# Kernel tuning notes

Hardware: AMD Instinct MI355X
Metric: run time of the kernel (lower is better)

Reference implementation:

```python
import jax, jax.numpy as jnp
import numpy as np

H = 16  # nhead


def setup_inputs() -> dict:
    key = jax.random.key(0)
    ks = jax.random.split(key, 10)
    B, N, D = 2, 2048, 1024
    n_ctx = 1024
    P = 256
    s = lambda fan: 1.0 / np.sqrt(fan)
    return {
        "x": jax.random.normal(ks[0], (B, N, D), jnp.float32),
        "n_ctx": n_ctx,
        "ctx_ppr": jax.random.uniform(ks[1], (n_ctx,), jnp.float32),
        "ctx_delta": jax.random.normal(ks[2], (n_ctx, P), jnp.float32),
        "ctx_trust": jax.random.normal(ks[3], (n_ctx,), jnp.float32),
        "W_in": jax.random.normal(ks[4], (3 * D, D), jnp.float32) * s(D),
        "b_in": jnp.zeros((3 * D,), jnp.float32),
        "W_out": jax.random.normal(ks[5], (D, D), jnp.float32) * s(D),
        "b_out": jnp.zeros((D,), jnp.float32),
        "log_ppr_alpha": jnp.full((1,), 0.1, jnp.float32),
        "trust_scale": jnp.full((1,), 0.1, jnp.float32),
        "Wd1": jax.random.normal(ks[6], (D // 2, P), jnp.float32) * s(P),
        "bd1": jnp.zeros((D // 2,), jnp.float32),
        "Wd2": jax.random.normal(ks[7], (1, D // 2), jnp.float32) * 0.01,
        "bd2": jnp.zeros((1,), jnp.float32),
    }


def reference(x, n_ctx, ctx_ppr, ctx_delta, ctx_trust, W_in, b_in, W_out, b_out,
              log_ppr_alpha, trust_scale, Wd1, bd1, Wd2, bd2):
    B, N, D = x.shape
    d = D // H
    scale = d ** -0.5

    qkv = x @ W_in.T + b_in                       # [B,N,3D]
    q, k, v = jnp.split(qkv, 3, axis=-1)
    to_heads = lambda t: t.reshape(B, N, H, d).transpose(0, 2, 1, 3)  # [B,H,N,d]
    q, k, v = to_heads(q), to_heads(k), to_heads(v)

    # sigmoid value gate on context keys
    gate = jax.nn.sigmoid(trust_scale * ctx_trust)           # [n_ctx]
    gate_full = jnp.concatenate([gate, jnp.ones(N - n_ctx, x.dtype)])
    v = v * gate_full[None, None, :, None]

    logits = jnp.einsum('bhqd,bhkd->bhqk', q, k) * scale     # [B,H,N,N]

    # additive per-key bias: alpha*log(ppr) + delta MLP
    ppr_bias = log_ppr_alpha * jnp.log(jnp.clip(ctx_ppr, 1e-8))
    h = jax.nn.gelu(ctx_delta @ Wd1.T + bd1, approximate=False)
    delta_bias = (h @ Wd2.T + bd2)[:, 0]                     # [n_ctx]
    col_bias = jnp.concatenate([ppr_bias + delta_bias, jnp.zeros(N - n_ctx, x.dtype)])
    logits = logits + col_bias[None, None, None, :]

    weights = jax.nn.softmax(logits, axis=-1)
    out = jnp.einsum('bhqk,bhkd->bhqd', weights, v)
    out = out.transpose(0, 2, 1, 3).reshape(B, N, D)
    return out @ W_out.T + b_out
```

## Files before the change

kernel.cpp:

```cpp
#include <hip/hip_runtime.h>
#include <hip/hip_bf16.h>
#include <hip/hip_fp16.h>
#include <math.h>


#define NTOK 2048
#define DMODEL 1024
#define NHEAD 16
#define DHEAD 64
#define NCTX 1024
#define BTOT 4096

typedef __attribute__((ext_vector_type(8))) _Float16 h8v;
typedef __attribute__((ext_vector_type(4))) float    f4v;
typedef __attribute__((ext_vector_type(4))) ushort   us4;
typedef __attribute__((ext_vector_type(8))) ushort   us8;

__device__ __forceinline__ ushort f2h(float x) {
    return __half_as_ushort(__float2half_rn(x));
}

#define GLDS16(gsrc, ldst) __builtin_amdgcn_global_load_lds(                              \
    (__attribute__((address_space(1))) unsigned int*)(gsrc),                              \
    (__attribute__((address_space(3))) unsigned int*)(ldst), 16, 0, 0)

__global__ __launch_bounds__(256)
void bias_kernel(const float* __restrict__ ctx_ppr, const float* __restrict__ ctx_delta,
                 const float* __restrict__ ctx_trust,
                 const float* __restrict__ alpha, const float* __restrict__ tscale,
                 const float* __restrict__ Wd1, const float* __restrict__ bd1,
                 const float* __restrict__ Wd2, const float* __restrict__ bd2,
                 float* __restrict__ gate_full, float* __restrict__ col_bias)
{
    const int i = blockIdx.x;
    const int t = threadIdx.x;
    if (i >= NCTX) {
        if (t == 0) { gate_full[i] = 1.0f; col_bias[i] = 0.0f; }
        return;
    }
    __shared__ float drow[256];
    __shared__ float red[256];
    drow[t] = ctx_delta[i * 256 + t];
    __syncthreads();

    float partial = 0.0f;
    #pragma unroll
    for (int jj = 0; jj < 2; jj++) {
        const int j = t + jj * 256;
        float s = bd1[j];
        const float4* wrow = (const float4*)&Wd1[j * 256];
        const float4* dr   = (const float4*)drow;
        #pragma unroll 8
        for (int p = 0; p < 64; p++) {
            float4 w = wrow[p], dd = dr[p];
            s += w.x * dd.x + w.y * dd.y + w.z * dd.z + w.w * dd.w;
        }
        float g = 0.5f * s * (1.0f + erff(s * 0.70710678118654752f));
        partial += g * Wd2[j];
    }
    red[t] = partial;
    __syncthreads();
    for (int off = 128; off > 0; off >>= 1) {
        if (t < off) red[t] += red[t + off];
        __syncthreads();
    }
    if (t == 0) {
        float ppr = fmaxf(ctx_ppr[i], 1e-8f);
        col_bias[i]  = alpha[0] * logf(ppr) + (red[0] + bd2[0]);
        gate_full[i] = 1.0f / (1.0f + __expf(-(tscale[0] * ctx_trust[i])));
    }
}

__global__ __launch_bounds__(256)
void cvt_all(const float* __restrict__ x, const float* __restrict__ wi,
             const float* __restrict__ wo,
             ushort* __restrict__ xf, ushort* __restrict__ wif, ushort* __restrict__ wof)
{
    for (int i = blockIdx.x * 256 + threadIdx.x; i < 2097152; i += gridDim.x * 256) {
        const float* src; ushort* dst; int j;
        if (i < 1048576)      { src = x;  dst = xf;  j = i; }
        else if (i < 1835008) { src = wi; dst = wif; j = i - 1048576; }
        else                  { src = wo; dst = wof; j = i - 1835008; }
        float4 v = ((const float4*)src)[j];
        us4 h;
        h[0] = f2h(v.x); h[1] = f2h(v.y); h[2] = f2h(v.z); h[3] = f2h(v.w);
        ((us4*)dst)[j] = h;
    }
}

template<int MT, int EPI>
__global__ __launch_bounds__(256, 3)
void gemm_f16(const ushort* __restrict__ Af, const ushort* __restrict__ Bf,
              const float* __restrict__ bias, float* __restrict__ C,
              ushort* __restrict__ qf, ushort* __restrict__ kf,
              ushort* __restrict__ vtf,
              const float* __restrict__ gate_full, int M, int N, int K)
{
    constexpr int BM = MT * 32;
    __shared__ ushort AS[BM * 32], BS[4096];

    const int t = threadIdx.x, lane = t & 63, wid = t >> 6;
    const int l15 = lane & 15, l4 = lane >> 4;
    const int wr = wid >> 1, wc = wid & 1;

    const int nwg = gridDim.x * gridDim.y;
    const int lin = blockIdx.y * gridDim.x + blockIdx.x;
    const int w   = (lin & 7) * (nwg >> 3) + (lin >> 3);
    const int bx  = w % gridDim.x, by = w / gridDim.x;
    const int m0 = by * BM, n0 = bx * 128;

    f4v acc[MT][4];
    #pragma unroll
    for (int mi = 0; mi < MT; mi++)
        #pragma unroll
        for (int nj = 0; nj < 4; nj++)
            #pragma unroll
            for (int r = 0; r < 4; r++) acc[mi][nj][r] = 0.0f;

    const int srow_l = lane >> 2;
    const int schunk = (lane & 3) ^ ((lane >> 2) & 3) ^ ((lane >> 4) & 3);
    const int rch = l4 ^ (l15 & 3) ^ ((l15 >> 2) & 3);

    for (int k0 = 0; k0 < K; k0 += 32) {
        __syncthreads();
        if (wid < 2) {
            #pragma unroll
            for (int i = 0; i < MT; i++) {
                const int row = (wid & 1) * (MT * 16) + i * 16 + srow_l;
                GLDS16(Af + (size_t)(m0 + row) * K + k0 + schunk * 8,
                       AS + ((wid & 1) * MT + i) * 512);
            }
        } else {
            #pragma unroll
            for (int i = 0; i < 4; i++) {
                const int row = (wid & 1) * 64 + i * 16 + srow_l;
                GLDS16(Bf + (size_t)(n0 + row) * K + k0 + schunk * 8,
                       BS + ((wid & 1) * 4 + i) * 512);
            }
        }
        __syncthreads();

        h8v af[MT], bf[4];
        #pragma unroll
        for (int mi = 0; mi < MT; mi++) {
            const int row = wr * (MT * 16) + mi * 16 + l15;
            af[mi] = *(const h8v*)&AS[row * 32 + rch * 8];
        }
        #pragma unroll
        for (int nj = 0; nj < 4; nj++) {
            const int row = wc * 64 + nj * 16 + l15;
            bf[nj] = *(const h8v*)&BS[row * 32 + rch * 8];
        }
        #pragma unroll
        for (int mi = 0; mi < MT; mi++)
            #pragma unroll
            for (int nj = 0; nj < 4; nj++)
                acc[mi][nj] = __builtin_amdgcn_mfma_f32_16x16x32_f16(af[mi], bf[nj], acc[mi][nj], 0, 0, 0);
    }

    if (EPI == 0) {
        #pragma unroll
        for (int mi = 0; mi < MT; mi++) {
            #pragma unroll
            for (int nj = 0; nj < 4; nj++) {
                const int n = n0 + wc * 64 + nj * 16 + l15;
                const float bn = bias[n];
                #pragma unroll
                for (int r = 0; r < 4; r++) {
                    const int m = m0 + wr * (MT * 16) + mi * 16 + l4 * 4 + r;
                    C[(size_t)m * N + n] = acc[mi][nj][r] + bn;
                }
            }
        }
    } else {
        const int sec = n0 >> 10;
        #pragma unroll
        for (int mi = 0; mi < MT; mi++) {
            const int mbase = m0 + wr * (MT * 16) + mi * 16 + l4 * 4;
            const int bb = mbase >> 11, tok0 = mbase & 2047;
            #pragma unroll
            for (int nj = 0; nj < 4; nj++) {
                const int n = n0 + wc * 64 + nj * 16 + l15;
                const float bn = bias[n];
                const int rem = n & 1023, h = rem >> 6, jd = rem & 63;
                if (sec == 2) {
                    us4 hv;
                    #pragma unroll
                    for (int r = 0; r < 4; r++)
                        hv[r] = f2h((acc[mi][nj][r] + bn) * gate_full[tok0 + r]);
                    const size_t vb = ((size_t)((bb << 4) + h) * 64 + jd) * NTOK + tok0;
                    *(us4*)&vtf[vb] = hv;
                } else {
                    ushort* dst = sec ? kf : qf;
                    #pragma unroll
                    for (int r = 0; r < 4; r++) {
                        const size_t idx = ((size_t)((bb << 4) + h) * NTOK + (tok0 + r)) * 64 + jd;
                        dst[idx] = f2h(acc[mi][nj][r] + bn);
                    }
                }
            }
        }
    }
}

__global__ __launch_bounds__(256, 4)
void attn_f16(const ushort* __restrict__ qfp, const ushort* __restrict__ kfp,
              const ushort* __restrict__ vtf, const float* __restrict__ col_bias,
              ushort* __restrict__ attf)
{
    __shared__ ushort KS[2][4096];
    __shared__ ushort VS[2][4096];
    __shared__ float  CBS[2][64];

    const int t = threadIdx.x, lane = t & 63, wid = t >> 6;
    const int lin = blockIdx.y * gridDim.x + blockIdx.x;
    const int w   = (lin & 7) * 128 + (lin >> 3);
    const int bh  = w >> 5, qt = w & 31;

    const size_t qkbase = (size_t)bh * (NTOK * DHEAD);
    const size_t vtbase = (size_t)bh * (DHEAD * NTOK);
    const int l15 = lane & 15, l4 = lane >> 4;
    const int q0 = qt * 64 + wid * 16;

    h8v qf[2];
    #pragma unroll
    for (int s = 0; s < 2; s++)
        qf[s] = *(const h8v*)&qfp[qkbase + (size_t)(q0 + l15) * 64 + 32 * s + 8 * l4];

    f4v oacc[4];
    #pragma unroll
    for (int f = 0; f < 4; f++)
        #pragma unroll
        for (int r = 0; r < 4; r++) oacc[f][r] = 0.0f;
    float mreg = -INFINITY;
    float sreg = 0.0f;

    us8 vreg[4];
    const int vj = lane & 7, vdh0 = lane >> 3;
    const int k0c  = 4 * (vj >> 2) + 2 * (vj & 1);
    const int off0 = ((vj >> 1) & 1) * 8;

    #define STAGE_K(nb, kt) do {                                                          \
        _Pragma("unroll")                                                                 \
        for (int i_ = 0; i_ < 4; i_++) {                                                  \
            const int row_ = wid * 32 + i_ * 8 + (lane >> 3);                             \
            const int sc_  = ((lane & 7) ^ (row_ & 7)) * 8;                               \
            GLDS16(kfp + qkbase + (size_t)((kt) + row_) * 64 + sc_,                       \
                   &KS[nb][0] + (wid * 4 + i_) * 512);                                    \
        }                                                                                 \
        if (wid == 0 && lane < 16) GLDS16(col_bias + (kt) + lane * 4, &CBS[nb][0]);       \
    } while (0)

    #define LOAD_V(kt) do {                                                               \
        _Pragma("unroll")                                                                 \
        for (int i_ = 0; i_ < 4; i_++) {                                                  \
            const int dh_ = (wid - 2) * 32 + 8 * i_ + vdh0;                               \
            vreg[i_] = *(const us8*)&vtf[vtbase + (size_t)dh_ * NTOK + (kt) + 8 * vj];    \
        }                                                                                 \
    } while (0)

    #define STORE_V(nb) do {                                                              \
        char* dp_ = (char*)&VS[nb][0];                                                    \
        _Pragma("unroll")                                                                 \
        for (int i_ = 0; i_ < 4; i_++) {                                                  \
            const int dh_ = (wid - 2) * 32 + 8 * i_ + vdh0;                               \
            const int b0_ = dh_ * 128 + ((k0c ^ (dh_ & 7)) * 16) + off0;                  \
            const int b1_ = dh_ * 128 + (((k0c + 1) ^ (dh_ & 7)) * 16) + off0;            \
            us4 lo4_, hi4_;                                                               \
            lo4_[0] = vreg[i_][0]; lo4_[1] = vreg[i_][1];                                 \
            lo4_[2] = vreg[i_][2]; lo4_[3] = vreg[i_][3];                                 \
            hi4_[0] = vreg[i_][4]; hi4_[1] = vreg[i_][5];                                 \
            hi4_[2] = vreg[i_][6]; hi4_[3] = vreg[i_][7];                                 \
            *(us4*)(dp_ + b0_) = lo4_;                                                    \
            *(us4*)(dp_ + b1_) = hi4_;                                                    \
        }                                                                                 \
    } while (0)

    if (wid < 2) STAGE_K(0, 0); else { LOAD_V(0); STORE_V(0); }
    __syncthreads();

    int cur = 0;
    for (int kt = 0; kt < 32; kt++) {
        const int nxt = cur ^ 1;
        if (kt < 31) { if (wid < 2) STAGE_K(nxt, (kt + 1) * 64); else LOAD_V((kt + 1) * 64); }

        f4v sa[4];
        #pragma unroll
        for (int g = 0; g < 4; g++)
            #pragma unroll
            for (int r = 0; r < 4; r++) sa[g][r] = 0.0f;
        __builtin_amdgcn_s_setprio(1);
        #pragma unroll
        for (int s = 0; s < 2; s++) {
            #pragma unroll
            for (int g = 0; g < 4; g++) {
                const int row = 16 * g + l15;
                const int idx = row * 64 + (((4 * s + l4) ^ (l15 & 7))) * 8;
                h8v kfr = *(const h8v*)&KS[cur][idx];
                sa[g] = __builtin_amdgcn_mfma_f32_16x16x32_f16(kfr, qf[s], sa[g], 0, 0, 0);
            }
        }
        __builtin_amdgcn_s_setprio(0);

        float sv[4][4], smax = -INFINITY;
        #pragma unroll
        for (int g = 0; g < 4; g++)
            #pragma unroll
            for (int r = 0; r < 4; r++) {
                const float x = sa[g][r] * 0.125f + CBS[cur][16 * g + 4 * l4 + r];
                sv[g][r] = x;
                smax = fmaxf(smax, x);
            }
        if (__any(smax > mreg + 8.0f)) {
            float mx = smax;
            mx = fmaxf(mx, __shfl_xor(mx, 16));
            mx = fmaxf(mx, __shfl_xor(mx, 32));
            const float mnew = fmaxf(mreg, mx);
            const float fs = __expf(mreg - mnew);
            mreg = mnew;
            sreg *= fs;
            float fq[4];
            #pragma unroll
            for (int r = 0; r < 4; r++) fq[r] = __shfl(fs, 4 * l4 + r);
            #pragma unroll
            for (int f = 0; f < 4; f++)
                #pragma unroll
                for (int r = 0; r < 4; r++) oacc[f][r] *= fq[r];
        }

        union H8 { h8v v; __half2 h2[4]; };
        H8 pa[2];
        {
            float pv[4][4];
            float acc_s = 0.0f;
            #pragma unroll
            for (int g = 0; g < 4; g++)
                #pragma unroll
                for (int r = 0; r < 4; r++) {
                    const float p = __expf(sv[g][r] - mreg);
                    pv[g][r] = p;
                    acc_s += p;
                }
            sreg += acc_s;
            #pragma unroll
            for (int s = 0; s < 2; s++)
                #pragma unroll
                for (int a = 0; a < 2; a++) {
                    const int g = 2 * s + a;
                    pa[s].h2[2 * a]     = __float22half2_rn(make_float2(pv[g][0], pv[g][1]));
                    pa[s].h2[2 * a + 1] = __float22half2_rn(make_float2(pv[g][2], pv[g][3]));
                }
        }

        __builtin_amdgcn_s_setprio(1);
        #pragma unroll
        for (int s = 0; s < 2; s++) {
            #pragma unroll
            for (int f = 0; f < 4; f++) {
                const int row = 16 * f + l15;
                const int idx = row * 64 + (((4 * s + l4) ^ (l15 & 7))) * 8;
                h8v vfr = *(const h8v*)&VS[cur][idx];
                oacc[f] = __builtin_amdgcn_mfma_f32_16x16x32_f16(pa[s].v, vfr, oacc[f], 0, 0, 0);
            }
        }
        __builtin_amdgcn_s_setprio(0);

        if (kt < 31 && wid >= 2) STORE_V(nxt);
        __syncthreads();
        cur = nxt;
    }

    const int b = bh >> 4, h = bh & 15;
    {
        float ts = sreg;
        ts += __shfl_xor(ts, 16);
        ts += __shfl_xor(ts, 32);
        const float inv = 1.0f / ts;
        float invq[4];
        #pragma unroll
        for (int r = 0; r < 4; r++) invq[r] = __shfl(inv, 4 * l4 + r);
        #pragma unroll
        for (int r = 0; r < 4; r++) {
            const int q = q0 + 4 * l4 + r;
            const size_t o = ((size_t)(b * NTOK + q)) * DMODEL + h * DHEAD + l15;
            #pragma unroll
            for (int f = 0; f < 4; f++)
                attf[o + 16 * f] = f2h(oacc[f][r] * invq[r]);
        }
    }
    #undef STAGE_K
    #undef LOAD_V
    #undef STORE_V
}

extern "C" void kernel_launch(void* const* d_in, const int* in_sizes, int n_in,
                              void* d_out, int out_size, void* d_ws, size_t ws_size,
                              hipStream_t stream)
{
    const float* x         = (const float*)d_in[0];
    const float* ctx_ppr   = (const float*)d_in[2];
    const float* ctx_delta = (const float*)d_in[3];
    const float* ctx_trust = (const float*)d_in[4];
    const float* W_in      = (const float*)d_in[5];
    const float* b_in      = (const float*)d_in[6];
    const float* W_out     = (const float*)d_in[7];
    const float* b_out     = (const float*)d_in[8];
    const float* alpha     = (const float*)d_in[9];
    const float* tscale    = (const float*)d_in[10];
    const float* Wd1       = (const float*)d_in[11];
    const float* bd1       = (const float*)d_in[12];
    const float* Wd2       = (const float*)d_in[13];
    const float* bd2       = (const float*)d_in[14];
    float* out = (float*)d_out;

    float* ws = (float*)d_ws;
    float* gate_full = ws;
    float* col_bias  = ws + 2048;
    ushort* u = (ushort*)(ws + 4096);
    ushort* xf   = u;  u += 4194304;
    ushort* wif  = u;  u += 3145728;
    ushort* wof  = u;  u += 1048576;
    ushort* qf   = u;  u += 4194304;
    ushort* kf   = u;  u += 4194304;
    ushort* vtf  = u;  u += 4194304;
    ushort* attf = u;  u += 4194304;

    bias_kernel<<<NTOK, 256, 0, stream>>>(ctx_ppr, ctx_delta, ctx_trust, alpha, tscale,
                                          Wd1, bd1, Wd2, bd2, gate_full, col_bias);
    cvt_all<<<2048, 256, 0, stream>>>(x, W_in, W_out, xf, wif, wof);

    gemm_f16<4, 1><<<dim3(24, 32), 256, 0, stream>>>(xf, wif, b_in, nullptr,
                                                     qf, kf, vtf, gate_full,
                                                     BTOT, 3 * DMODEL, DMODEL);
    attn_f16<<<dim3(32, 32), 256, 0, stream>>>(qf, kf, vtf, col_bias, attf);
    gemm_f16<2, 0><<<dim3(8, 64), 256, 0, stream>>>(attf, wof, b_out, out,
                                                    nullptr, nullptr, nullptr, nullptr,
                                                    BTOT, DMODEL, DMODEL);
}
```

Baseline: 275.2 us.

## Use exp2 softmax, MFMA row sums, trimmed bias launch, smaller out-proj tiles

```diff
diff --git a/kernel.cpp b/kernel.cpp
--- a/kernel.cpp
+++ b/kernel.cpp
@@ -10,6 +10,7 @@
 #define DHEAD 64
 #define NCTX 1024
 #define BTOT 4096
+#define LOG2E 1.4426950408889634f
 
 typedef __attribute__((ext_vector_type(8))) _Float16 h8v;
 typedef __attribute__((ext_vector_type(4))) float    f4v;
@@ -19,6 +20,12 @@
 __device__ __forceinline__ ushort f2h(float x) {
     return __half_as_ushort(__float2half_rn(x));
 }
+
+#if __has_builtin(__builtin_amdgcn_exp2f)
+#define EXP2F(x) __builtin_amdgcn_exp2f(x)
+#else
+#define EXP2F(x) exp2f(x)
+#endif
 
 #define GLDS16(gsrc, ldst) __builtin_amdgcn_global_load_lds(                              \
     (__attribute__((address_space(1))) unsigned int*)(gsrc),                              \
@@ -34,10 +41,6 @@
 {
     const int i = blockIdx.x;
     const int t = threadIdx.x;
-    if (i >= NCTX) {
-        if (t == 0) { gate_full[i] = 1.0f; col_bias[i] = 0.0f; }
-        return;
-    }
     __shared__ float drow[256];
     __shared__ float red[256];
     drow[t] = ctx_delta[i * 256 + t];
@@ -66,7 +69,7 @@
     }
     if (t == 0) {
         float ppr = fmaxf(ctx_ppr[i], 1e-8f);
-        col_bias[i]  = alpha[0] * logf(ppr) + (red[0] + bd2[0]);
+        col_bias[i]  = (alpha[0] * logf(ppr) + (red[0] + bd2[0])) * LOG2E;
         gate_full[i] = 1.0f / (1.0f + __expf(-(tscale[0] * ctx_trust[i])));
     }
 }
@@ -74,8 +77,16 @@
 __global__ __launch_bounds__(256)
 void cvt_all(const float* __restrict__ x, const float* __restrict__ wi,
              const float* __restrict__ wo,
-             ushort* __restrict__ xf, ushort* __restrict__ wif, ushort* __restrict__ wof)
+             ushort* __restrict__ xf, ushort* __restrict__ wif, ushort* __restrict__ wof,
+             float* __restrict__ gate_full, float* __restrict__ col_bias)
 {
+    if (blockIdx.x == 0) {
+        #pragma unroll
+        for (int j = threadIdx.x; j < NTOK - NCTX; j += 256) {
+            gate_full[NCTX + j] = 1.0f;
+            col_bias[NCTX + j]  = 0.0f;
+        }
+    }
     for (int i = blockIdx.x * 256 + threadIdx.x; i < 2097152; i += gridDim.x * 256) {
         const float* src; ushort* dst; int j;
         if (i < 1048576)      { src = x;  dst = xf;  j = i; }
@@ -227,13 +238,18 @@
     for (int s = 0; s < 2; s++)
         qf[s] = *(const h8v*)&qfp[qkbase + (size_t)(q0 + l15) * 64 + 32 * s + 8 * l4];
 
-    f4v oacc[4];
+    h8v vone;
+    #pragma unroll
+    for (int i = 0; i < 8; i++) vone[i] = (_Float16)1.0f;
+
+    f4v oacc[4], lsum;
     #pragma unroll
     for (int f = 0; f < 4; f++)
         #pragma unroll
         for (int r = 0; r < 4; r++) oacc[f][r] = 0.0f;
+    #pragma unroll
+    for (int r = 0; r < 4; r++) lsum[r] = 0.0f;
     float mreg = -INFINITY;
-    float sreg = 0.0f;
 
     us8 vreg[4];
     const int vj = lane & 7, vdh0 = lane >> 3;
@@ -302,26 +318,28 @@
         }
         __builtin_amdgcn_s_setprio(0);
 
+        const float SC2 = 0.125f * LOG2E;
         float sv[4][4], smax = -INFINITY;
         #pragma unroll
         for (int g = 0; g < 4; g++)
             #pragma unroll
             for (int r = 0; r < 4; r++) {
-                const float x = sa[g][r] * 0.125f + CBS[cur][16 * g + 4 * l4 + r];
+                const float x = sa[g][r] * SC2 + CBS[cur][16 * g + 4 * l4 + r];
                 sv[g][r] = x;
                 smax = fmaxf(smax, x);
             }
-        if (__any(smax > mreg + 8.0f)) {
+        if (__any(smax > mreg + 11.5415605f)) {
             float mx = smax;
             mx = fmaxf(mx, __shfl_xor(mx, 16));
             mx = fmaxf(mx, __shfl_xor(mx, 32));
             const float mnew = fmaxf(mreg, mx);
-            const float fs = __expf(mreg - mnew);
+            const float fs = EXP2F(mreg - mnew);
             mreg = mnew;
-            sreg *= fs;
             float fq[4];
             #pragma unroll
             for (int r = 0; r < 4; r++) fq[r] = __shfl(fs, 4 * l4 + r);
+            #pragma unroll
+            for (int r = 0; r < 4; r++) lsum[r] *= fq[r];
             #pragma unroll
             for (int f = 0; f < 4; f++)
                 #pragma unroll
@@ -332,16 +350,11 @@
         H8 pa[2];
         {
             float pv[4][4];
-            float acc_s = 0.0f;
             #pragma unroll
             for (int g = 0; g < 4; g++)
                 #pragma unroll
-                for (int r = 0; r < 4; r++) {
-                    const float p = __expf(sv[g][r] - mreg);
-                    pv[g][r] = p;
-                    acc_s += p;
-                }
-            sreg += acc_s;
+                for (int r = 0; r < 4; r++)
+                    pv[g][r] = EXP2F(sv[g][r] - mreg);
             #pragma unroll
             for (int s = 0; s < 2; s++)
                 #pragma unroll
@@ -355,6 +368,7 @@
         __builtin_amdgcn_s_setprio(1);
         #pragma unroll
         for (int s = 0; s < 2; s++) {
+            lsum = __builtin_amdgcn_mfma_f32_16x16x32_f16(pa[s].v, vone, lsum, 0, 0, 0);
             #pragma unroll
             for (int f = 0; f < 4; f++) {
                 const int row = 16 * f + l15;
@@ -371,22 +385,14 @@
     }
 
     const int b = bh >> 4, h = bh & 15;
-    {
-        float ts = sreg;
-        ts += __shfl_xor(ts, 16);
-        ts += __shfl_xor(ts, 32);
-        const float inv = 1.0f / ts;
-        float invq[4];
-        #pragma unroll
-        for (int r = 0; r < 4; r++) invq[r] = __shfl(inv, 4 * l4 + r);
-        #pragma unroll
-        for (int r = 0; r < 4; r++) {
-            const int q = q0 + 4 * l4 + r;
-            const size_t o = ((size_t)(b * NTOK + q)) * DMODEL + h * DHEAD + l15;
-            #pragma unroll
-            for (int f = 0; f < 4; f++)
-                attf[o + 16 * f] = f2h(oacc[f][r] * invq[r]);
-        }
+    #pragma unroll
+    for (int r = 0; r < 4; r++) {
+        const float inv = 1.0f / lsum[r];
+        const int q = q0 + 4 * l4 + r;
+        const size_t o = ((size_t)(b * NTOK + q)) * DMODEL + h * DHEAD + l15;
+        #pragma unroll
+        for (int f = 0; f < 4; f++)
+            attf[o + 16 * f] = f2h(oacc[f][r] * inv);
     }
     #undef STAGE_K
     #undef LOAD_V
@@ -425,15 +431,15 @@
     ushort* vtf  = u;  u += 4194304;
     ushort* attf = u;  u += 4194304;
 
-    bias_kernel<<<NTOK, 256, 0, stream>>>(ctx_ppr, ctx_delta, ctx_trust, alpha, tscale,
+    bias_kernel<<<NCTX, 256, 0, stream>>>(ctx_ppr, ctx_delta, ctx_trust, alpha, tscale,
                                           Wd1, bd1, Wd2, bd2, gate_full, col_bias);
-    cvt_all<<<2048, 256, 0, stream>>>(x, W_in, W_out, xf, wif, wof);
+    cvt_all<<<2048, 256, 0, stream>>>(x, W_in, W_out, xf, wif, wof, gate_full, col_bias);
 
     gemm_f16<4, 1><<<dim3(24, 32), 256, 0, stream>>>(xf, wif, b_in, nullptr,
                                                      qf, kf, vtf, gate_full,
                                                      BTOT, 3 * DMODEL, DMODEL);
     attn_f16<<<dim3(32, 32), 256, 0, stream>>>(qf, kf, vtf, col_bias, attf);
-    gemm_f16<2, 0><<<dim3(8, 64), 256, 0, stream>>>(attf, wof, b_out, out,
-                                                    nullptr, nullptr, nullptr, nullptr,
-                                                    BTOT, DMODEL, DMODEL);
-}
+    gemm_f16<1, 0><<<dim3(8, 128), 256, 0, stream>>>(attf, wof, b_out, out,
+                                                     nullptr, nullptr, nullptr, nullptr,
+                                                     BTOT, DMODEL, DMODEL);
+}
```

Measured after the change: 271.1 us. About the same (-1.5%).
